# Kernel tuning notes

Measured on AMD Instinct MI355X. Metric: run time of the kernel, lower is better.

## Reference

```python
import jax, jax.numpy as jnp
import numpy as np

PAD = 0  # padding token id; its embedding row is zero (padding_idx)


def setup_inputs() -> dict:
    key = jax.random.key(0)
    k1, k2, k3 = jax.random.split(key, 3)
    HOPS, VOCAB, D = 3, 50257, 128
    B, M, S = 32, 512, 6        # batch, memory slots, tokens per slot
    T, L = 128, 64              # trees per example, tokens per (flattened) tree
    # hop+1 embedding tables, normal(0, 0.1) like the torch init
    C = 0.1 * jax.random.normal(k1, (HOPS + 1, VOCAB, D), dtype=jnp.float32)
    C = C.at[:, PAD].set(0.0)   # padding_idx row = 0
    story = jax.random.randint(k2, (B, M, S), 0, VOCAB, dtype=jnp.int32)
    kb_tokens = jax.random.randint(k3, (B, T, L), 0, VOCAB, dtype=jnp.int32)
    return {"C": C, "story": story, "kb_tokens": kb_tokens}


def reference(C, story, kb_tokens):
    # C: [hops+1, V, D]; story: [B, M, S]; kb_tokens: [B, T, L]
    hops = C.shape[0] - 1
    B = story.shape[0]
    D = C.shape[-1]
    u = jnp.zeros((B, D), dtype=C.dtype)
    for hop in range(hops):
        # key memory: story slots (sum over tokens) + tree memories (sum over
        # all subtree tokens == dfs recursive sum, since PAD embeds to zero)
        m_story_A = jnp.take(C[hop], story, axis=0).sum(axis=2)       # [B,M,D]
        tree_A = jnp.take(C[hop], kb_tokens, axis=0).sum(axis=2)      # [B,T,D]
        m_A = jnp.concatenate([m_story_A, tree_A], axis=1)            # [B,M+T,D]
        prob = jax.nn.softmax(jnp.einsum("bmd,bd->bm", m_A, u), axis=1)
        # value memory with next-hop table
        m_story_C = jnp.take(C[hop + 1], story, axis=0).sum(axis=2)
        tree_C = jnp.take(C[hop + 1], kb_tokens, axis=0).sum(axis=2)
        m_C = jnp.concatenate([m_story_C, tree_C], axis=1)
        o_k = jnp.einsum("bm,bmd->bd", prob, m_C)
        u = u + o_k
    return u
```

## Files before the change

### kernel.cpp

```cpp
#include <hip/hip_runtime.h>
#include <math.h>

constexpr int HOPS  = 3;
constexpr int VOCAB = 50257;
constexpr int DIM   = 128;
constexpr int NB    = 32;
constexpr int NM    = 512;
constexpr int NS    = 6;
constexpr int NT    = 128;
constexpr int NL    = 64;
constexpr int SLOTS = NM + NT;
constexpr size_t TS = (size_t)VOCAB * DIM;
constexpr size_t TABSTRIDE = (size_t)NB * SLOTS * DIM;

constexpr size_t CH_ELEMS = (size_t)VOCAB * 3 * DIM;
constexpr int NE8 = (int)(CH_ELEMS / 8);

typedef _Float16 half8 __attribute__((ext_vector_type(8)));
typedef _Float16 half4 __attribute__((ext_vector_type(4)));

constexpr int CONV_BLOCKS  = 2048;
constexpr int STORY_BLOCKS = 2048;
constexpr int K1_BLOCKS    = CONV_BLOCKS + STORY_BLOCKS;
constexpr int TREE_BLOCKS  = NB * NT / 4;

__device__ __forceinline__ void addf4(float4& a, const float4& v) {
    a.x += v.x; a.y += v.y; a.z += v.z; a.w += v.w;
}

__global__ __launch_bounds__(256) void convert_story_k(
    const float* __restrict__ C, const int* __restrict__ story,
    _Float16* __restrict__ Ch, _Float16* __restrict__ msum)
{
    if (blockIdx.x & 1) {
        const int sb   = blockIdx.x >> 1;
        const int wave = threadIdx.x >> 6, lane = threadIdx.x & 63;
        const int h = lane >> 5, l32 = lane & 31;
        const int g = sb * 8 + wave * 2 + h;
        const int b = g >> 9, slot = g & (NM - 1);

        const int* idx = story + (size_t)g * NS;
        const int tokv = (l32 < NS) ? idx[l32] : 0;

        const float* Cb = C + TS + (size_t)l32 * 4;
        float4 a0 = {0,0,0,0}, a1 = {0,0,0,0}, a2 = {0,0,0,0};
        #pragma unroll
        for (int i = 0; i < NS; ++i) {
            const int s = __shfl(tokv, h * 32 + i);
            const float* p = Cb + (size_t)s * DIM;
            addf4(a0, *(const float4*)(p));
            addf4(a1, *(const float4*)(p + TS));
            addf4(a2, *(const float4*)(p + 2 * TS));
        }
        half4 h0, h1, h2;
        h0[0]=(_Float16)a0.x; h0[1]=(_Float16)a0.y; h0[2]=(_Float16)a0.z; h0[3]=(_Float16)a0.w;
        h1[0]=(_Float16)a1.x; h1[1]=(_Float16)a1.y; h1[2]=(_Float16)a1.z; h1[3]=(_Float16)a1.w;
        h2[0]=(_Float16)a2.x; h2[1]=(_Float16)a2.y; h2[2]=(_Float16)a2.z; h2[3]=(_Float16)a2.w;
        const size_t o = ((size_t)b * SLOTS + slot) * DIM + l32 * 4;
        *(half4*)(msum + o)                 = h0;
        *(half4*)(msum + o + TABSTRIDE)     = h1;
        *(half4*)(msum + o + 2 * TABSTRIDE) = h2;
    } else {
        const int cb = blockIdx.x >> 1;
        for (int e8 = cb * 256 + threadIdx.x; e8 < NE8; e8 += CONV_BLOCKS * 256) {
            const size_t base = (size_t)e8 * 8;
            const size_t v    = base / 384;
            const int    rem  = (int)(base % 384);
            const int    tab  = rem >> 7;
            const int    d    = rem & 127;
            const float* src = C + (size_t)(1 + tab) * TS + v * DIM + d;
            float4 f0 = *(const float4*)(src);
            float4 f1 = *(const float4*)(src + 4);
            half8 h;
            h[0]=(_Float16)f0.x; h[1]=(_Float16)f0.y; h[2]=(_Float16)f0.z; h[3]=(_Float16)f0.w;
            h[4]=(_Float16)f1.x; h[5]=(_Float16)f1.y; h[6]=(_Float16)f1.z; h[7]=(_Float16)f1.w;
            *(half8*)(Ch + base) = h;
        }
    }
}

__global__ __launch_bounds__(256) void tree_gather(
    const _Float16* __restrict__ Ch, const int* __restrict__ kb,
    _Float16* __restrict__ msum)
{
    const int wave = threadIdx.x >> 6, lane = threadIdx.x & 63;
    const int q = lane >> 4, l16 = lane & 15;
    const int g = blockIdx.x * 4 + wave;
    const int b = g >> 7, tr = g & (NT - 1);

    const int tok = kb[(size_t)g * NL + lane];

    float a0[8] = {0,0,0,0,0,0,0,0};
    float a1[8] = {0,0,0,0,0,0,0,0};
    float a2[8] = {0,0,0,0,0,0,0,0};

    #pragma unroll
    for (int i = 0; i < 16; ++i) {
        const int s = __shfl(tok, (lane & 48) + i);
        const _Float16* p = Ch + (size_t)s * (3 * DIM) + l16 * 8;
        half8 v0 = *(const half8*)(p);
        half8 v1 = *(const half8*)(p + DIM);
        half8 v2 = *(const half8*)(p + 2 * DIM);
        #pragma unroll
        for (int j = 0; j < 8; ++j) {
            a0[j] += (float)v0[j];
            a1[j] += (float)v1[j];
            a2[j] += (float)v2[j];
        }
    }
    #pragma unroll
    for (int j = 0; j < 8; ++j) {
        a0[j] += __shfl_xor(a0[j], 16); a0[j] += __shfl_xor(a0[j], 32);
        a1[j] += __shfl_xor(a1[j], 16); a1[j] += __shfl_xor(a1[j], 32);
        a2[j] += __shfl_xor(a2[j], 16); a2[j] += __shfl_xor(a2[j], 32);
    }
    if (q == 0) {
        half8 h0, h1, h2;
        #pragma unroll
        for (int j = 0; j < 8; ++j) {
            h0[j] = (_Float16)a0[j]; h1[j] = (_Float16)a1[j]; h2[j] = (_Float16)a2[j];
        }
        const size_t o = ((size_t)b * SLOTS + NM + tr) * DIM + l16 * 8;
        *(half8*)(msum + o)                 = h0;
        *(half8*)(msum + o + TABSTRIDE)     = h1;
        *(half8*)(msum + o + 2 * TABSTRIDE) = h2;
    }
}

__global__ __launch_bounds__(1024) void hops_fused(
    const _Float16* __restrict__ msum, float* __restrict__ out)
{
    const int b = blockIdx.x, t = threadIdx.x;
    const int rg = t >> 4, l16 = t & 15, wv = t >> 6, ln = t & 63;
    __shared__ float u_s[DIM];
    __shared__ float probs[SLOTS];
    __shared__ float part[64][DIM + 4];
    __shared__ float red[16];

    const _Float16* base = msum + (size_t)b * SLOTS * DIM;

    {
        float acc[8] = {0,0,0,0,0,0,0,0};
        #pragma unroll
        for (int m = rg; m < SLOTS; m += 64) {
            half8 v = *(const half8*)(base + (size_t)m * DIM + l16 * 8);
            #pragma unroll
            for (int j = 0; j < 8; ++j) acc[j] += (float)v[j];
        }
        #pragma unroll
        for (int j = 0; j < 8; ++j) part[rg][l16 * 8 + j] = acc[j];
        __syncthreads();
        if (t < DIM) {
            float s = 0.f;
            #pragma unroll
            for (int r = 0; r < 64; ++r) s += part[r][t];
            u_s[t] = s * (1.f / SLOTS);
        }
        __syncthreads();
    }

    for (int hop = 1; hop < HOPS; ++hop) {
        const _Float16* mA = base + (size_t)(hop - 1) * TABSTRIDE;
        const _Float16* mC = base + (size_t)hop * TABSTRIDE;

        #pragma unroll
        for (int m = rg; m < SLOTS; m += 64) {
            half8 v = *(const half8*)(mA + (size_t)m * DIM + l16 * 8);
            float d = 0.f;
            #pragma unroll
            for (int j = 0; j < 8; ++j) d = fmaf((float)v[j], u_s[l16 * 8 + j], d);
            d += __shfl_xor(d, 1); d += __shfl_xor(d, 2);
            d += __shfl_xor(d, 4); d += __shfl_xor(d, 8);
            if (l16 == 0) probs[m] = d;
        }
        __syncthreads();

        float s0 = (t < SLOTS) ? probs[t] : -INFINITY;
        float lmax = s0;
        #pragma unroll
        for (int off = 32; off > 0; off >>= 1) lmax = fmaxf(lmax, __shfl_xor(lmax, off));
        if (ln == 0) red[wv] = lmax;
        __syncthreads();
        lmax = red[0];
        #pragma unroll
        for (int r = 1; r < 16; ++r) lmax = fmaxf(lmax, red[r]);
        __syncthreads();
        float e0 = (t < SLOTS) ? expf(s0 - lmax) : 0.f;
        if (t < SLOTS) probs[t] = e0;
        float lsum = e0;
        #pragma unroll
        for (int off = 32; off > 0; off >>= 1) lsum += __shfl_xor(lsum, off);
        if (ln == 0) red[wv] = lsum;
        __syncthreads();
        float tot = red[0];
        #pragma unroll
        for (int r = 1; r < 16; ++r) tot += red[r];
        const float inv = 1.0f / tot;

        float acc[8] = {0,0,0,0,0,0,0,0};
        #pragma unroll
        for (int m = rg; m < SLOTS; m += 64) {
            const float p = probs[m];
            half8 v = *(const half8*)(mC + (size_t)m * DIM + l16 * 8);
            #pragma unroll
            for (int j = 0; j < 8; ++j) acc[j] = fmaf(p, (float)v[j], acc[j]);
        }
        __syncthreads();
        #pragma unroll
        for (int j = 0; j < 8; ++j) part[rg][l16 * 8 + j] = acc[j];
        __syncthreads();
        if (t < DIM) {
            float s = 0.f;
            #pragma unroll
            for (int r = 0; r < 64; ++r) s += part[r][t];
            u_s[t] += s * inv;
        }
        __syncthreads();
    }

    if (t < DIM) out[b * DIM + t] = u_s[t];
}

extern "C" void kernel_launch(void* const* d_in, const int* in_sizes, int n_in,
                              void* d_out, int out_size, void* d_ws, size_t ws_size,
                              hipStream_t stream) {
    const float* C     = (const float*)d_in[0];
    const int*   story = (const int*)d_in[1];
    const int*   kb    = (const int*)d_in[2];
    float*       out   = (float*)d_out;

    _Float16* Ch   = (_Float16*)d_ws;
    _Float16* msum = Ch + CH_ELEMS;

    convert_story_k<<<K1_BLOCKS, 256, 0, stream>>>(C, story, Ch, msum);
    tree_gather<<<TREE_BLOCKS, 256, 0, stream>>>(Ch, kb, msum);
    hops_fused<<<NB, 1024, 0, stream>>>(msum, out);
}
```

Measured before the change: 214.0 us.

## Gather story slots from converted fp16 table in combined gather kernel

Story-slot gathering no longer reads the fp32 tables alongside the conversion. It now runs in a single gather kernel together with the tree gather and reads the interleaved fp16 table, with two waves per block on trees and two on story slots (four slots per wave). This halves the bytes fetched per story-slot gather and removes the mixed convert/gather kernel. The cost is that story gathering can no longer overlap the conversion and must wait for it. The plain adds were also rewritten as fmaf with 1.0, which changes nothing in substance.

```diff
diff --git a/kernel.cpp b/kernel.cpp
--- a/kernel.cpp
+++ b/kernel.cpp
@@ -19,108 +19,108 @@
 typedef _Float16 half8 __attribute__((ext_vector_type(8)));
 typedef _Float16 half4 __attribute__((ext_vector_type(4)));
 
-constexpr int CONV_BLOCKS  = 2048;
-constexpr int STORY_BLOCKS = 2048;
-constexpr int K1_BLOCKS    = CONV_BLOCKS + STORY_BLOCKS;
-constexpr int TREE_BLOCKS  = NB * NT / 4;
-
-__device__ __forceinline__ void addf4(float4& a, const float4& v) {
-    a.x += v.x; a.y += v.y; a.z += v.z; a.w += v.w;
-}
-
-__global__ __launch_bounds__(256) void convert_story_k(
-    const float* __restrict__ C, const int* __restrict__ story,
-    _Float16* __restrict__ Ch, _Float16* __restrict__ msum)
+constexpr int CONV_BLOCKS   = 2048;
+constexpr int GATHER_BLOCKS = 2048;
+
+__global__ __launch_bounds__(256) void convert_k(
+    const float* __restrict__ C, _Float16* __restrict__ Ch)
 {
-    if (blockIdx.x & 1) {
-        const int sb   = blockIdx.x >> 1;
-        const int wave = threadIdx.x >> 6, lane = threadIdx.x & 63;
-        const int h = lane >> 5, l32 = lane & 31;
-        const int g = sb * 8 + wave * 2 + h;
-        const int b = g >> 9, slot = g & (NM - 1);
-
-        const int* idx = story + (size_t)g * NS;
-        const int tokv = (l32 < NS) ? idx[l32] : 0;
-
-        const float* Cb = C + TS + (size_t)l32 * 4;
-        float4 a0 = {0,0,0,0}, a1 = {0,0,0,0}, a2 = {0,0,0,0};
-        #pragma unroll
-        for (int i = 0; i < NS; ++i) {
-            const int s = __shfl(tokv, h * 32 + i);
-            const float* p = Cb + (size_t)s * DIM;
-            addf4(a0, *(const float4*)(p));
-            addf4(a1, *(const float4*)(p + TS));
-            addf4(a2, *(const float4*)(p + 2 * TS));
-        }
-        half4 h0, h1, h2;
-        h0[0]=(_Float16)a0.x; h0[1]=(_Float16)a0.y; h0[2]=(_Float16)a0.z; h0[3]=(_Float16)a0.w;
-        h1[0]=(_Float16)a1.x; h1[1]=(_Float16)a1.y; h1[2]=(_Float16)a1.z; h1[3]=(_Float16)a1.w;
-        h2[0]=(_Float16)a2.x; h2[1]=(_Float16)a2.y; h2[2]=(_Float16)a2.z; h2[3]=(_Float16)a2.w;
-        const size_t o = ((size_t)b * SLOTS + slot) * DIM + l32 * 4;
-        *(half4*)(msum + o)                 = h0;
-        *(half4*)(msum + o + TABSTRIDE)     = h1;
-        *(half4*)(msum + o + 2 * TABSTRIDE) = h2;
-    } else {
-        const int cb = blockIdx.x >> 1;
-        for (int e8 = cb * 256 + threadIdx.x; e8 < NE8; e8 += CONV_BLOCKS * 256) {
-            const size_t base = (size_t)e8 * 8;
-            const size_t v    = base / 384;
-            const int    rem  = (int)(base % 384);
-            const int    tab  = rem >> 7;
-            const int    d    = rem & 127;
-            const float* src = C + (size_t)(1 + tab) * TS + v * DIM + d;
-            float4 f0 = *(const float4*)(src);
-            float4 f1 = *(const float4*)(src + 4);
-            half8 h;
-            h[0]=(_Float16)f0.x; h[1]=(_Float16)f0.y; h[2]=(_Float16)f0.z; h[3]=(_Float16)f0.w;
-            h[4]=(_Float16)f1.x; h[5]=(_Float16)f1.y; h[6]=(_Float16)f1.z; h[7]=(_Float16)f1.w;
-            *(half8*)(Ch + base) = h;
-        }
-    }
-}
-
-__global__ __launch_bounds__(256) void tree_gather(
-    const _Float16* __restrict__ Ch, const int* __restrict__ kb,
-    _Float16* __restrict__ msum)
+    for (int e8 = blockIdx.x * 256 + threadIdx.x; e8 < NE8; e8 += CONV_BLOCKS * 256) {
+        const size_t base = (size_t)e8 * 8;
+        const size_t v    = base / 384;
+        const int    rem  = (int)(base % 384);
+        const int    tab  = rem >> 7;
+        const int    d    = rem & 127;
+        const float* src = C + (size_t)(1 + tab) * TS + v * DIM + d;
+        float4 f0 = *(const float4*)(src);
+        float4 f1 = *(const float4*)(src + 4);
+        half8 h;
+        h[0]=(_Float16)f0.x; h[1]=(_Float16)f0.y; h[2]=(_Float16)f0.z; h[3]=(_Float16)f0.w;
+        h[4]=(_Float16)f1.x; h[5]=(_Float16)f1.y; h[6]=(_Float16)f1.z; h[7]=(_Float16)f1.w;
+        *(half8*)(Ch + base) = h;
+    }
+}
+
+__global__ __launch_bounds__(256) void gather_k(
+    const _Float16* __restrict__ Ch, const int* __restrict__ story,
+    const int* __restrict__ kb, _Float16* __restrict__ msum)
 {
     const int wave = threadIdx.x >> 6, lane = threadIdx.x & 63;
     const int q = lane >> 4, l16 = lane & 15;
-    const int g = blockIdx.x * 4 + wave;
-    const int b = g >> 7, tr = g & (NT - 1);
-
-    const int tok = kb[(size_t)g * NL + lane];
-
-    float a0[8] = {0,0,0,0,0,0,0,0};
-    float a1[8] = {0,0,0,0,0,0,0,0};
-    float a2[8] = {0,0,0,0,0,0,0,0};
-
-    #pragma unroll
-    for (int i = 0; i < 16; ++i) {
-        const int s = __shfl(tok, (lane & 48) + i);
-        const _Float16* p = Ch + (size_t)s * (3 * DIM) + l16 * 8;
-        half8 v0 = *(const half8*)(p);
-        half8 v1 = *(const half8*)(p + DIM);
-        half8 v2 = *(const half8*)(p + 2 * DIM);
+
+    if (wave < 2) {
+        const int g = blockIdx.x * 2 + wave;
+        const int b = g >> 7, tr = g & (NT - 1);
+
+        const int tok = kb[(size_t)g * NL + lane];
+
+        float a0[8] = {0,0,0,0,0,0,0,0};
+        float a1[8] = {0,0,0,0,0,0,0,0};
+        float a2[8] = {0,0,0,0,0,0,0,0};
+
+        #pragma unroll
+        for (int i = 0; i < 16; ++i) {
+            const int s = __shfl(tok, (lane & 48) + i);
+            const _Float16* p = Ch + (size_t)s * (3 * DIM) + l16 * 8;
+            half8 v0 = *(const half8*)(p);
+            half8 v1 = *(const half8*)(p + DIM);
+            half8 v2 = *(const half8*)(p + 2 * DIM);
+            #pragma unroll
+            for (int j = 0; j < 8; ++j) {
+                a0[j] = fmaf((float)v0[j], 1.0f, a0[j]);
+                a1[j] = fmaf((float)v1[j], 1.0f, a1[j]);
+                a2[j] = fmaf((float)v2[j], 1.0f, a2[j]);
+            }
+        }
         #pragma unroll
         for (int j = 0; j < 8; ++j) {
-            a0[j] += (float)v0[j];
-            a1[j] += (float)v1[j];
-            a2[j] += (float)v2[j];
-        }
-    }
-    #pragma unroll
-    for (int j = 0; j < 8; ++j) {
-        a0[j] += __shfl_xor(a0[j], 16); a0[j] += __shfl_xor(a0[j], 32);
-        a1[j] += __shfl_xor(a1[j], 16); a1[j] += __shfl_xor(a1[j], 32);
-        a2[j] += __shfl_xor(a2[j], 16); a2[j] += __shfl_xor(a2[j], 32);
-    }
-    if (q == 0) {
+            a0[j] += __shfl_xor(a0[j], 16); a0[j] += __shfl_xor(a0[j], 32);
+            a1[j] += __shfl_xor(a1[j], 16); a1[j] += __shfl_xor(a1[j], 32);
+            a2[j] += __shfl_xor(a2[j], 16); a2[j] += __shfl_xor(a2[j], 32);
+        }
+        if (q == 0) {
+            half8 h0, h1, h2;
+            #pragma unroll
+            for (int j = 0; j < 8; ++j) {
+                h0[j] = (_Float16)a0[j]; h1[j] = (_Float16)a1[j]; h2[j] = (_Float16)a2[j];
+            }
+            const size_t o = ((size_t)b * SLOTS + NM + tr) * DIM + l16 * 8;
+            *(half8*)(msum + o)                 = h0;
+            *(half8*)(msum + o + TABSTRIDE)     = h1;
+            *(half8*)(msum + o + 2 * TABSTRIDE) = h2;
+        }
+    } else {
+        const int wbase = blockIdx.x * 8 + (wave - 2) * 4;
+        const int* sidx = story + (size_t)wbase * NS;
+        const int tokv = (lane < 4 * NS) ? sidx[lane] : 0;
+
+        const int g = wbase + q;
+        const int b = g >> 9, slot = g & (NM - 1);
+
+        float a0[8] = {0,0,0,0,0,0,0,0};
+        float a1[8] = {0,0,0,0,0,0,0,0};
+        float a2[8] = {0,0,0,0,0,0,0,0};
+
+        #pragma unroll
+        for (int i = 0; i < NS; ++i) {
+            const int s = __shfl(tokv, q * NS + i);
+            const _Float16* p = Ch + (size_t)s * (3 * DIM) + l16 * 8;
+            half8 v0 = *(const half8*)(p);
+            half8 v1 = *(const half8*)(p + DIM);
+            half8 v2 = *(const half8*)(p + 2 * DIM);
+            #pragma unroll
+            for (int j = 0; j < 8; ++j) {
+                a0[j] = fmaf((float)v0[j], 1.0f, a0[j]);
+                a1[j] = fmaf((float)v1[j], 1.0f, a1[j]);
+                a2[j] = fmaf((float)v2[j], 1.0f, a2[j]);
+            }
+        }
         half8 h0, h1, h2;
         #pragma unroll
         for (int j = 0; j < 8; ++j) {
             h0[j] = (_Float16)a0[j]; h1[j] = (_Float16)a1[j]; h2[j] = (_Float16)a2[j];
         }
-        const size_t o = ((size_t)b * SLOTS + NM + tr) * DIM + l16 * 8;
+        const size_t o = ((size_t)b * SLOTS + slot) * DIM + l16 * 8;
         *(half8*)(msum + o)                 = h0;
         *(half8*)(msum + o + TABSTRIDE)     = h1;
         *(half8*)(msum + o + 2 * TABSTRIDE) = h2;
@@ -232,7 +232,7 @@
     _Float16* Ch   = (_Float16*)d_ws;
     _Float16* msum = Ch + CH_ELEMS;
 
-    convert_story_k<<<K1_BLOCKS, 256, 0, stream>>>(C, story, Ch, msum);
-    tree_gather<<<TREE_BLOCKS, 256, 0, stream>>>(Ch, kb, msum);
+    convert_k<<<CONV_BLOCKS, 256, 0, stream>>>(C, Ch);
+    gather_k<<<GATHER_BLOCKS, 256, 0, stream>>>(Ch, story, kb, msum);
     hops_fused<<<NB, 1024, 0, stream>>>(msum, out);
 }
```

After: 211.2 us (median of 2 runs). No clear change (-1.3%).
